# Performance work log

Hardware: AMD Instinct MI355X
Metric: run time of the kernel (lower is better)

## Reference

```python
import jax, jax.numpy as jnp
import numpy as np

Q_DIM = 512
K_DIM = 512
HID = 512


def setup_inputs() -> dict:
    key = jax.random.key(0)
    k1, k2, k3, k4, k5, k6 = jax.random.split(key, 6)
    b, n_q, s = 4, 64, 1024
    queries = jax.random.normal(k1, (b, n_q, Q_DIM), dtype=jnp.float32)
    keys = jax.random.normal(k2, (b, s, K_DIM), dtype=jnp.float32)
    values = jax.random.normal(k3, (b, s, 512), dtype=jnp.float32)
    lim1 = 1.0 / np.sqrt(Q_DIM + K_DIM)
    W1 = jax.random.uniform(k4, (HID, Q_DIM + K_DIM), minval=-lim1, maxval=lim1, dtype=jnp.float32)
    b1 = jax.random.uniform(k5, (HID,), minval=-lim1, maxval=lim1, dtype=jnp.float32)
    lim2 = 1.0 / np.sqrt(HID)
    w2 = jax.random.uniform(k6, (HID,), minval=-lim2, maxval=lim2, dtype=jnp.float32)
    return {"queries": queries, "keys": keys, "values": values,
            "W1": W1, "b1": b1, "w2": w2}


def reference(queries, keys, values, W1, b1, w2):
    # linear1 on concat([q, k]) == W1q @ q + W1k @ k (split the weight),
    # avoiding materializing the concatenated [b, n_q, s, q_v+k_v] tensor.
    W1q = W1[:, :Q_DIM]  # [hid, q_dim]
    W1k = W1[:, Q_DIM:]  # [hid, k_dim]
    q_proj = jnp.einsum('bqd,hd->bqh', queries, W1q)          # [b, n_q, hid]
    k_proj = jnp.einsum('bsd,hd->bsh', keys, W1k) + b1        # [b, s, hid]
    hidden = jnp.tanh(q_proj[:, :, None, :] + k_proj[:, None, :, :])  # [b, n_q, s, hid]
    scores = jnp.einsum('bqsh,h->bqs', hidden, w2)            # [b, n_q, s]
    attn = jax.nn.softmax(scores, axis=2)                     # softmax over key axis
    final = jnp.einsum('bqs,bsv->bqv', attn, values)          # [b, n_q, v_dim]
    return final
```

## Files before the change

### kernel.cpp

```cpp
#include <hip/hip_runtime.h>


static constexpr int SLEN = 1024;
static constexpr int DIM  = 512;
static constexpr float TANH_SCALE = 2.885390081777927f;

typedef __attribute__((ext_vector_type(8))) short bf16x8;
typedef __attribute__((ext_vector_type(4))) float f32x4;

__device__ __forceinline__ float fast_exp2(float x) { return __builtin_amdgcn_exp2f(x); }
__device__ __forceinline__ float fast_rcp(float x)  { return __builtin_amdgcn_rcpf(x); }

__device__ __forceinline__ unsigned int f2bf(float f) {
    unsigned int u = __float_as_uint(f);
    u += 0x7FFF + ((u >> 16) & 1);
    return u >> 16;
}

__device__ __forceinline__ void async_copy16(const void* g, void* l) {
    __builtin_amdgcn_global_load_lds(
        (const __attribute__((address_space(1))) unsigned int*)g,
        (__attribute__((address_space(3))) unsigned int*)l, 16, 0, 0);
}

__global__ __launch_bounds__(256) void convert_bf16(
    const float* __restrict__ q, const float* __restrict__ k,
    const float* __restrict__ w, unsigned short* __restrict__ qb,
    unsigned short* __restrict__ kb, unsigned short* __restrict__ wb)
{
    int id = blockIdx.x * 256 + threadIdx.x;
    const float* src; unsigned short* dst; int off;
    if (id < 32768)        { src = q; dst = qb; off = id; }
    else if (id < 557056)  { src = k; dst = kb; off = id - 32768; }
    else                   { src = w; dst = wb; off = id - 557056; }
    float4 v = ((const float4*)src)[off];
    ushort4 o;
    o.x = (unsigned short)f2bf(v.x); o.y = (unsigned short)f2bf(v.y);
    o.z = (unsigned short)f2bf(v.z); o.w = (unsigned short)f2bf(v.w);
    ((ushort4*)dst)[off] = o;
}

__global__ __launch_bounds__(256) void proj_mfma(
    const unsigned short* __restrict__ qb, const unsigned short* __restrict__ kb,
    const unsigned short* __restrict__ wb, const float* __restrict__ b1,
    float* __restrict__ qp, float* __restrict__ kp)
{
    __shared__ __align__(16) unsigned short As[64][64];
    __shared__ __align__(16) unsigned short Ws[64][64];

    const int bx = blockIdx.x;
    const unsigned short* A; float* C; const float* bias; int mb, nb, col_off;
    if (bx < 512) {
        A = kb; C = kp; bias = b1; col_off = 512;
        mb = (bx >> 3) * 64; nb = (bx & 7) * 64;
    } else {
        int b2 = bx - 512;
        A = qb; C = qp; bias = nullptr; col_off = 0;
        mb = (b2 >> 3) * 64; nb = (b2 & 7) * 64;
    }

    const int t = threadIdx.x;
    const int l = t & 63;
    const int wv = t >> 6;
    const int wm = (wv & 1) * 32;
    const int wn = (wv >> 1) * 32;
    const int lane16 = l & 15;
    const int quad   = l >> 4;
    const int r8   = l >> 3;
    const int schk = (l & 7) ^ r8;

    f32x4 acc[2][2] = {{{0.f,0.f,0.f,0.f},{0.f,0.f,0.f,0.f}},
                       {{0.f,0.f,0.f,0.f},{0.f,0.f,0.f,0.f}}};

    for (int kc = 0; kc < DIM; kc += 64) {
#pragma unroll
        for (int i = 0; i < 2; ++i) {
            int rbase = wv * 16 + i * 8;
            async_copy16(A + (size_t)(mb + rbase + r8) * DIM + kc + schk * 8, &As[rbase][0]);
            async_copy16(wb + (size_t)(nb + rbase + r8) * 1024 + col_off + kc + schk * 8, &Ws[rbase][0]);
        }
        __syncthreads();

#pragma unroll
        for (int ks = 0; ks < 2; ++ks) {
            int cc = ks * 4 + quad;
            int sw = (cc ^ (lane16 & 7)) << 3;
            bf16x8 a0  = *(const bf16x8*)&As[wm + lane16][sw];
            bf16x8 a1  = *(const bf16x8*)&As[wm + 16 + lane16][sw];
            bf16x8 b0  = *(const bf16x8*)&Ws[wn + lane16][sw];
            bf16x8 b1v = *(const bf16x8*)&Ws[wn + 16 + lane16][sw];
            acc[0][0] = __builtin_amdgcn_mfma_f32_16x16x32_bf16(a0, b0,  acc[0][0], 0, 0, 0);
            acc[0][1] = __builtin_amdgcn_mfma_f32_16x16x32_bf16(a0, b1v, acc[0][1], 0, 0, 0);
            acc[1][0] = __builtin_amdgcn_mfma_f32_16x16x32_bf16(a1, b0,  acc[1][0], 0, 0, 0);
            acc[1][1] = __builtin_amdgcn_mfma_f32_16x16x32_bf16(a1, b1v, acc[1][1], 0, 0, 0);
        }
        __syncthreads();
    }

#pragma unroll
    for (int mi = 0; mi < 2; ++mi) {
#pragma unroll
        for (int ni = 0; ni < 2; ++ni) {
            int col = nb + wn + 16 * ni + lane16;
            float bv = bias ? bias[col] : 0.0f;
#pragma unroll
            for (int r = 0; r < 4; ++r) {
                int row = mb + wm + 16 * mi + quad * 4 + r;
                C[(size_t)row * DIM + col] = (acc[mi][ni][r] + bv) * TANH_SCALE;
            }
        }
    }
}

__global__ __launch_bounds__(256) void scores_kernel(
    const float* __restrict__ qp, const float* __restrict__ kp,
    const float* __restrict__ w2, float* __restrict__ th)
{
    __shared__ __align__(16) float qs[16][68];
    __shared__ __align__(16) float ks[32][68];
    __shared__ __align__(16) float ws2[128];
    const int t     = threadIdx.x;
    const int sb    = blockIdx.x * 32;
    const int qt    = blockIdx.y & 3;
    const int qu    = blockIdx.y >> 2;
    const int kbase = qu * 128;
    const int qrow0 = blockIdx.z * 64 + qt * 16;
    const int krow0 = blockIdx.z * 1024 + sb;
    float* thh = th + (size_t)qu * 256 * SLEN;

    if (t < 32) *(float4*)&ws2[t << 2] = *(const float4*)(w2 + kbase + (t << 2));

    const int tq = t >> 4;
    const int ts = t & 15;
    float a00 = 0.f, a01 = 0.f, a10 = 0.f, a11 = 0.f;

    for (int kc = 0; kc < 128; kc += 64) {
        {
            int r = t >> 4, g = (t & 15) << 2;
            *(float4*)&qs[r][g] = *(const float4*)(qp + (size_t)(qrow0 + r) * DIM + kbase + kc + g);
        }
#pragma unroll
        for (int rr = 0; rr < 2; ++rr) {
            int idx = t + rr * 256;
            int r = idx >> 4, g = (idx & 15) << 2;
            *(float4*)&ks[r][g] = *(const float4*)(kp + (size_t)(krow0 + r) * DIM + kbase + kc + g);
        }
        __syncthreads();
#pragma unroll
        for (int k4 = 0; k4 < 16; ++k4) {
            float4 qv = *(const float4*)&qs[tq][k4 << 2];
            float4 k0 = *(const float4*)&ks[ts][k4 << 2];
            float4 k1 = *(const float4*)&ks[ts + 16][k4 << 2];
            float4 wv = *(const float4*)&ws2[kc + (k4 << 2)];
            a00 = fmaf(wv.x, fast_rcp(1.0f + fast_exp2(qv.x + k0.x)), a00);
            a10 = fmaf(wv.x, fast_rcp(1.0f + fast_exp2(qv.x + k1.x)), a10);
            a01 = fmaf(wv.y, fast_rcp(1.0f + fast_exp2(qv.y + k0.y)), a01);
            a11 = fmaf(wv.y, fast_rcp(1.0f + fast_exp2(qv.y + k1.y)), a11);
            a00 = fmaf(wv.z, fast_rcp(1.0f + fast_exp2(qv.z + k0.z)), a00);
            a10 = fmaf(wv.z, fast_rcp(1.0f + fast_exp2(qv.z + k1.z)), a10);
            a01 = fmaf(wv.w, fast_rcp(1.0f + fast_exp2(qv.w + k0.w)), a01);
            a11 = fmaf(wv.w, fast_rcp(1.0f + fast_exp2(qv.w + k1.w)), a11);
        }
        __syncthreads();
    }
    thh[(size_t)(qrow0 + tq) * SLEN + sb + ts]      = -TANH_SCALE * (a00 + a01);
    thh[(size_t)(qrow0 + tq) * SLEN + sb + ts + 16] = -TANH_SCALE * (a10 + a11);
}

__global__ __launch_bounds__(256) void av_gemm(
    const float* __restrict__ th, const float* __restrict__ values,
    float* __restrict__ pt, float* __restrict__ sums_p)
{
    __shared__ __align__(16) float As[32][68];
    __shared__ __align__(16) float Bs[32][68];
    const int t  = threadIdx.x;
    const int nb = blockIdx.x * 64;
    const int kt = blockIdx.y;
    const int kb = kt * 128;
    const int b  = blockIdx.z;
    const int tx = t & 15, ty = t >> 4;
    float acc[4][4] = {};
    float rsum[2] = {0.f, 0.f};
    for (int kc = 0; kc < 128; kc += 32) {
        const int k0 = kb + kc;
#pragma unroll
        for (int r = 0; r < 2; ++r) {
            int idx = t + r * 256;
            int m   = idx >> 3;
            int k4  = (idx & 7) << 2;
            size_t base = (size_t)(b * 64 + m) * SLEN + k0 + k4;
            float4 t0 = *(const float4*)(th + base);
            float4 t1 = *(const float4*)(th + 262144 + base);
            float4 t2 = *(const float4*)(th + 524288 + base);
            float4 t3 = *(const float4*)(th + 786432 + base);
            float4 e;
            e.x = fast_exp2(t0.x + t1.x + t2.x + t3.x);
            e.y = fast_exp2(t0.y + t1.y + t2.y + t3.y);
            e.z = fast_exp2(t0.z + t1.z + t2.z + t3.z);
            e.w = fast_exp2(t0.w + t1.w + t2.w + t3.w);
            As[k4 + 0][m] = e.x; As[k4 + 1][m] = e.y;
            As[k4 + 2][m] = e.z; As[k4 + 3][m] = e.w;
            rsum[r] += e.x + e.y + e.z + e.w;
            int kk = idx >> 4;
            int g  = (idx & 15) << 2;
            *(float4*)&Bs[kk][g] =
                *(const float4*)(values + (size_t)(b * 1024 + k0 + kk) * DIM + nb + g);
        }
        __syncthreads();
#pragma unroll
        for (int k = 0; k < 32; ++k) {
            float4 a  = *(const float4*)&As[k][ty << 2];
            float4 bv = *(const float4*)&Bs[k][tx << 2];
            float am[4] = {a.x, a.y, a.z, a.w};
            float bn[4] = {bv.x, bv.y, bv.z, bv.w};
#pragma unroll
            for (int i = 0; i < 4; ++i)
#pragma unroll
                for (int j = 0; j < 4; ++j)
                    acc[i][j] = fmaf(am[i], bn[j], acc[i][j]);
        }
        __syncthreads();
    }
#pragma unroll
    for (int i = 0; i < 4; ++i) {
        int row = b * 64 + (ty << 2) + i;
        float4 o;
        o.x = acc[i][0]; o.y = acc[i][1]; o.z = acc[i][2]; o.w = acc[i][3];
        *(float4*)(pt + ((size_t)kt * 256 + row) * DIM + nb + (tx << 2)) = o;
    }
    if (nb == 0) {
#pragma unroll
        for (int r = 0; r < 2; ++r) {
            float v = rsum[r];
            v += __shfl_xor(v, 1, 64);
            v += __shfl_xor(v, 2, 64);
            v += __shfl_xor(v, 4, 64);
            if ((t & 7) == 0) {
                int m = (t >> 3) + r * 32;
                sums_p[kt * 256 + b * 64 + m] = v;
            }
        }
    }
}

__global__ __launch_bounds__(256) void reduce_kernel(
    const float* __restrict__ pt, const float* __restrict__ sums_p,
    float* __restrict__ out)
{
    int idx = blockIdx.x * 256 + threadIdx.x;
    const float4* p = (const float4*)pt;
    float4 a = p[idx];
#pragma unroll
    for (int k = 1; k < 8; ++k) {
        float4 v = p[k * 32768 + idx];
        a.x += v.x; a.y += v.y; a.z += v.z; a.w += v.w;
    }
    int row = idx >> 7;
    float s = 0.f;
#pragma unroll
    for (int k = 0; k < 8; ++k) s += sums_p[k * 256 + row];
    float r = fast_rcp(s);
    a.x *= r; a.y *= r; a.z *= r; a.w *= r;
    ((float4*)out)[idx] = a;
}

extern "C" void kernel_launch(void* const* d_in, const int* in_sizes, int n_in,
                              void* d_out, int out_size, void* d_ws, size_t ws_size,
                              hipStream_t stream) {
    const float* queries = (const float*)d_in[0];
    const float* keys    = (const float*)d_in[1];
    const float* values  = (const float*)d_in[2];
    const float* W1      = (const float*)d_in[3];
    const float* b1      = (const float*)d_in[4];
    const float* w2      = (const float*)d_in[5];
    float* out = (float*)d_out;

    float* qp     = (float*)d_ws;
    float* kp     = qp + 131072;
    float* th     = kp + 2097152;
    float* pt     = th + 4 * 262144;
    float* sums_p = pt + 8 * 131072;
    unsigned short* qbf = (unsigned short*)(sums_p + 2048);
    unsigned short* kbf = qbf + 131072;
    unsigned short* wbf = kbf + 2097152;
    (void)in_sizes; (void)n_in; (void)ws_size; (void)out_size;

    convert_bf16<<<dim3(2688), 256, 0, stream>>>(queries, keys, W1, qbf, kbf, wbf);
    proj_mfma<<<dim3(544), 256, 0, stream>>>(qbf, kbf, wbf, b1, qp, kp);
    scores_kernel<<<dim3(32, 16, 4), 256, 0, stream>>>(qp, kp, w2, th);
    av_gemm<<<dim3(8, 8, 4), 256, 0, stream>>>(th, values, pt, sums_p);
    reduce_kernel<<<dim3(128), 256, 0, stream>>>(pt, sums_p, out);
}
```

Before: 128.5 us.

## Pair sigmoid reciprocals and halve hidden-dim split of the scores kernel

The scores kernel now combines two sigmoid terms over a common denominator, so one reciprocal serves two hidden units and the number of rcp instructions is halved. It also splits the hidden dimension into 2 partitions of 256 instead of 4 of 128. That halves the partial-score buffer written by scores_kernel and read by av_gemm, and halves the score-kernel grid. The trade-offs are fewer blocks in flight, longer per-block loops, and a risk of overflow or precision loss when the product of two exp2 terms gets very large.

Result: faster. 122.7 us (-4.6%).

```diff
diff --git a/kernel.cpp b/kernel.cpp
--- a/kernel.cpp
+++ b/kernel.cpp
@@ -118,23 +118,23 @@
 {
     __shared__ __align__(16) float qs[16][68];
     __shared__ __align__(16) float ks[32][68];
-    __shared__ __align__(16) float ws2[128];
+    __shared__ __align__(16) float ws2[256];
     const int t     = threadIdx.x;
     const int sb    = blockIdx.x * 32;
     const int qt    = blockIdx.y & 3;
-    const int qu    = blockIdx.y >> 2;
-    const int kbase = qu * 128;
+    const int half  = blockIdx.y >> 2;
+    const int kbase = half * 256;
     const int qrow0 = blockIdx.z * 64 + qt * 16;
     const int krow0 = blockIdx.z * 1024 + sb;
-    float* thh = th + (size_t)qu * 256 * SLEN;
-
-    if (t < 32) *(float4*)&ws2[t << 2] = *(const float4*)(w2 + kbase + (t << 2));
+    float* thh = th + (size_t)half * 256 * SLEN;
+
+    if (t < 64) *(float4*)&ws2[t << 2] = *(const float4*)(w2 + kbase + (t << 2));
 
     const int tq = t >> 4;
     const int ts = t & 15;
     float a00 = 0.f, a01 = 0.f, a10 = 0.f, a11 = 0.f;
 
-    for (int kc = 0; kc < 128; kc += 64) {
+    for (int kc = 0; kc < 256; kc += 64) {
         {
             int r = t >> 4, g = (t & 15) << 2;
             *(float4*)&qs[r][g] = *(const float4*)(qp + (size_t)(qrow0 + r) * DIM + kbase + kc + g);
@@ -152,14 +152,30 @@
             float4 k0 = *(const float4*)&ks[ts][k4 << 2];
             float4 k1 = *(const float4*)&ks[ts + 16][k4 << 2];
             float4 wv = *(const float4*)&ws2[kc + (k4 << 2)];
-            a00 = fmaf(wv.x, fast_rcp(1.0f + fast_exp2(qv.x + k0.x)), a00);
-            a10 = fmaf(wv.x, fast_rcp(1.0f + fast_exp2(qv.x + k1.x)), a10);
-            a01 = fmaf(wv.y, fast_rcp(1.0f + fast_exp2(qv.y + k0.y)), a01);
-            a11 = fmaf(wv.y, fast_rcp(1.0f + fast_exp2(qv.y + k1.y)), a11);
-            a00 = fmaf(wv.z, fast_rcp(1.0f + fast_exp2(qv.z + k0.z)), a00);
-            a10 = fmaf(wv.z, fast_rcp(1.0f + fast_exp2(qv.z + k1.z)), a10);
-            a01 = fmaf(wv.w, fast_rcp(1.0f + fast_exp2(qv.w + k0.w)), a01);
-            a11 = fmaf(wv.w, fast_rcp(1.0f + fast_exp2(qv.w + k1.w)), a11);
+            {
+                float dx = 1.0f + fast_exp2(qv.x + k0.x);
+                float dy = 1.0f + fast_exp2(qv.y + k0.y);
+                float num = fmaf(wv.y, dx, wv.x * dy);
+                a00 = fmaf(num, fast_rcp(dx * dy), a00);
+            }
+            {
+                float dz = 1.0f + fast_exp2(qv.z + k0.z);
+                float dw = 1.0f + fast_exp2(qv.w + k0.w);
+                float num = fmaf(wv.w, dz, wv.z * dw);
+                a01 = fmaf(num, fast_rcp(dz * dw), a01);
+            }
+            {
+                float dx = 1.0f + fast_exp2(qv.x + k1.x);
+                float dy = 1.0f + fast_exp2(qv.y + k1.y);
+                float num = fmaf(wv.y, dx, wv.x * dy);
+                a10 = fmaf(num, fast_rcp(dx * dy), a10);
+            }
+            {
+                float dz = 1.0f + fast_exp2(qv.z + k1.z);
+                float dw = 1.0f + fast_exp2(qv.w + k1.w);
+                float num = fmaf(wv.w, dz, wv.z * dw);
+                a11 = fmaf(num, fast_rcp(dz * dw), a11);
+            }
         }
         __syncthreads();
     }
@@ -191,13 +207,11 @@
             size_t base = (size_t)(b * 64 + m) * SLEN + k0 + k4;
             float4 t0 = *(const float4*)(th + base);
             float4 t1 = *(const float4*)(th + 262144 + base);
-            float4 t2 = *(const float4*)(th + 524288 + base);
-            float4 t3 = *(const float4*)(th + 786432 + base);
             float4 e;
-            e.x = fast_exp2(t0.x + t1.x + t2.x + t3.x);
-            e.y = fast_exp2(t0.y + t1.y + t2.y + t3.y);
-            e.z = fast_exp2(t0.z + t1.z + t2.z + t3.z);
-            e.w = fast_exp2(t0.w + t1.w + t2.w + t3.w);
+            e.x = fast_exp2(t0.x + t1.x);
+            e.y = fast_exp2(t0.y + t1.y);
+            e.z = fast_exp2(t0.z + t1.z);
+            e.w = fast_exp2(t0.w + t1.w);
             As[k4 + 0][m] = e.x; As[k4 + 1][m] = e.y;
             As[k4 + 2][m] = e.z; As[k4 + 3][m] = e.w;
             rsum[r] += e.x + e.y + e.z + e.w;
@@ -278,7 +292,7 @@
     float* qp     = (float*)d_ws;
     float* kp     = qp + 131072;
     float* th     = kp + 2097152;
-    float* pt     = th + 4 * 262144;
+    float* pt     = th + 2 * 262144;
     float* sums_p = pt + 8 * 131072;
     unsigned short* qbf = (unsigned short*)(sums_p + 2048);
     unsigned short* kbf = qbf + 131072;
@@ -287,7 +301,7 @@
 
     convert_bf16<<<dim3(2688), 256, 0, stream>>>(queries, keys, W1, qbf, kbf, wbf);
     proj_mfma<<<dim3(544), 256, 0, stream>>>(qbf, kbf, wbf, b1, qp, kp);
-    scores_kernel<<<dim3(32, 16, 4), 256, 0, stream>>>(qp, kp, w2, th);
+    scores_kernel<<<dim3(32, 8, 4), 256, 0, stream>>>(qp, kp, w2, th);
     av_gemm<<<dim3(8, 8, 4), 256, 0, stream>>>(th, values, pt, sums_p);
     reduce_kernel<<<dim3(128), 256, 0, stream>>>(pt, sums_p, out);
 }
```
